# Kernel optimization log

Hardware: AMD Instinct MI355X
Metric: run time of the kernel (lower is better)

## Reference

```python
import jax, jax.numpy as jnp
import numpy as np

EPS = 1e-12  # torch F.normalize eps


def _unfold(x, k, pad, stride):
    # torch F.unfold: [B,C,H,W] -> [B, C*k*k, L], channel-major then kernel (i,j)
    B, C, H, W = x.shape
    xp = jnp.pad(x, ((0, 0), (0, 0), (pad, pad), (pad, pad)))
    Ho = (H + 2 * pad - k) // stride + 1
    Wo = (W + 2 * pad - k) // stride + 1
    patches = [xp[:, :, i:i + stride * (Ho - 1) + 1:stride, j:j + stride * (Wo - 1) + 1:stride]
               for i in range(k) for j in range(k)]
    p = jnp.stack(patches, axis=2)  # [B, C, k*k, Ho, Wo]
    return p.reshape(B, C * k * k, Ho * Wo)


def _fold(t, out_hw, k, pad, stride):
    # torch F.fold: [B, C*k*k, L] -> [B, C, H, W] with overlap-add
    B, Ckk, L = t.shape
    C = Ckk // (k * k)
    H, W = out_hw
    Ho = (H + 2 * pad - k) // stride + 1
    Wo = (W + 2 * pad - k) // stride + 1
    t = t.reshape(B, C, k, k, Ho, Wo)
    out = jnp.zeros((B, C, H + 2 * pad, W + 2 * pad), t.dtype)
    for i in range(k):
        for j in range(k):
            out = out.at[:, :, i:i + stride * (Ho - 1) + 1:stride,
                         j:j + stride * (Wo - 1) + 1:stride].add(t[:, :, i, j])
    return out[:, :, pad:pad + H, pad:pad + W]


def setup_inputs() -> dict:
    key = jax.random.key(0)
    ks = jax.random.split(key, 5)
    B, C3, H3 = 4, 256, 48
    return {
        'dh_img_lv3': jax.random.normal(ks[0], (B, C3, H3, H3), jnp.float32),
        'dh_ref_lv3': jax.random.normal(ks[1], (B, C3, H3, H3), jnp.float32),
        'cl_ref_lv1': jax.random.normal(ks[2], (B, 64, H3 * 4, H3 * 4), jnp.float32),
        'cl_ref_lv2': jax.random.normal(ks[3], (B, 128, H3 * 2, H3 * 2), jnp.float32),
        'cl_ref_lv3': jax.random.normal(ks[4], (B, C3, H3, H3), jnp.float32),
    }


def reference(dh_img_lv3, dh_ref_lv3, cl_ref_lv1, cl_ref_lv2, cl_ref_lv3):
    ksz, pad = 3, 1
    B, C3, H3, W3 = dh_img_lv3.shape

    q = _unfold(dh_img_lv3, ksz, pad, 1)                      # [B, D, Lq]
    kmat = _unfold(dh_ref_lv3, ksz, pad, 1).transpose(0, 2, 1)  # [B, Lk, D]
    kmat = kmat / jnp.maximum(jnp.linalg.norm(kmat, axis=2, keepdims=True), EPS)
    q = q / jnp.maximum(jnp.linalg.norm(q, axis=1, keepdims=True), EPS)

    rel = jnp.einsum('bld,bdm->blm', kmat, q)                 # [B, Lk, Lq]
    rel_val = jnp.max(rel, axis=1, keepdims=True)             # [B, 1, Lq]  (top-1, k=1)
    rel_idx = jnp.argmax(rel, axis=1, keepdims=True)          # [B, 1, Lq]

    v3 = _unfold(cl_ref_lv3, ksz, pad, 1)                     # [B, C3*9,   Lk]
    v2 = _unfold(cl_ref_lv2, 2 * ksz, 2 * pad, 2)             # [B, C2*36,  Lk]
    v1 = _unfold(cl_ref_lv1, 4 * ksz, 4 * pad, 4)             # [B, C1*144, Lk]

    def transfer(v):
        idx = jnp.broadcast_to(rel_idx, (B, v.shape[1], rel_idx.shape[2]))
        tv = jnp.take_along_axis(v, idx, axis=2)              # [B, Cv, Lq]
        # weighted sum over k=1 topk / sum of weights (faithful to original)
        return (rel_val * tv) / rel_val

    T3u, T2u, T1u = transfer(v3), transfer(v2), transfer(v1)

    def fold_norm(Tu, scale, k_, p_, s_):
        hw = (H3 * scale, W3 * scale)
        cnt = _fold(jnp.ones_like(Tu), hw, k_, p_, s_)
        return _fold(Tu, hw, k_, p_, s_) / cnt

    T_lv3 = fold_norm(T3u, 1, ksz, pad, 1)
    T_lv2 = fold_norm(T2u, 2, 2 * ksz, 2 * pad, 2)
    T_lv1 = fold_norm(T1u, 4, 4 * ksz, 4 * pad, 4)

    S = rel_val.reshape(B, 1, H3, W3)
    return S, T_lv3, T_lv2, T_lv1
```

## Files before the change

kernel.cpp:

```cpp
#include <hip/hip_runtime.h>


#define HW3 2304
#define PLANE 589824
#define SSTRIDE 5308416LL

__global__ __launch_bounds__(256) void k_pixsq(const float* __restrict__ img,
                                               const float* __restrict__ ref,
                                               float* __restrict__ psi,
                                               float* __restrict__ psr) {
  __shared__ float ri[16][17], rr[16][17];
  int t = threadIdx.x;
  int pl = t & 15, cg = t >> 4;
  int pix = blockIdx.x * 16 + pl;
  int b = pix / HW3, p = pix - b * HW3;
  const float* ib = img + (size_t)b * PLANE + p;
  const float* rb = ref + (size_t)b * PLANE + p;
  float si = 0.f, sr = 0.f;
#pragma unroll
  for (int c = 0; c < 16; ++c) {
    float x = ib[(cg * 16 + c) * HW3]; si = fmaf(x, x, si);
    float y = rb[(cg * 16 + c) * HW3]; sr = fmaf(y, y, sr);
  }
  ri[pl][cg] = si; rr[pl][cg] = sr;
  __syncthreads();
  if (t < 16) {
    float a = 0.f, s2 = 0.f;
#pragma unroll
    for (int g = 0; g < 16; ++g) { a += ri[t][g]; s2 += rr[t][g]; }
    int pix2 = blockIdx.x * 16 + t;
    psi[pix2] = a; psr[pix2] = s2;
  }
}

__global__ __launch_bounds__(256) void k_norm(const float* __restrict__ psr,
                                              const float* __restrict__ psi,
                                              float* __restrict__ ikn,
                                              float* __restrict__ iqn) {
  int pix = blockIdx.x * 256 + threadIdx.x;
  int b = pix / HW3, p = pix - b * HW3;
  int py = p / 48, px = p - py * 48;
  float sr = 0.f, si = 0.f;
#pragma unroll
  for (int dy = -1; dy <= 1; ++dy) {
#pragma unroll
    for (int dx = -1; dx <= 1; ++dx) {
      if (py + dy < 0 || py + dy >= 48 || px + dx < 0 || px + dx >= 48) continue;
      int n = pix + dy * 48 + dx;
      sr += psr[n]; si += psi[n];
    }
  }
  ikn[pix] = 1.0f / fmaxf(sqrtf(sr), 1e-12f);
  iqn[pix] = 1.0f / fmaxf(sqrtf(si), 1e-12f);
}

__global__ __launch_bounds__(256) void k_gemm(const float* __restrict__ img,
                                              const float* __restrict__ ref,
                                              float* __restrict__ S,
                                              int b0, long long sstride) {
  __shared__ float As[8][128];
  __shared__ float Bs[8][128];
  const float* A  = img + (size_t)(b0 + blockIdx.z) * PLANE;
  const float* Bm = ref + (size_t)(b0 + blockIdx.z) * PLANE;
  float* Sb = S + (size_t)blockIdx.z * sstride;
  const int t = threadIdx.x;
  const int q0 = blockIdx.y * 128, p0 = blockIdx.x * 128;
  const int lr = t >> 5, lc = (t & 31) << 2;
  const int tq = t >> 4, tp = t & 15;
  float acc[8][8];
#pragma unroll
  for (int u = 0; u < 8; ++u)
#pragma unroll
    for (int v = 0; v < 8; ++v) acc[u][v] = 0.f;

  for (int c0 = 0; c0 < 256; c0 += 8) {
    float4 a4 = *(const float4*)(A  + (c0 + lr) * HW3 + q0 + lc);
    float4 b4 = *(const float4*)(Bm + (c0 + lr) * HW3 + p0 + lc);
    __syncthreads();
    *(float4*)(&As[lr][lc]) = a4;
    *(float4*)(&Bs[lr][lc]) = b4;
    __syncthreads();
#pragma unroll
    for (int kk = 0; kk < 8; ++kk) {
      float4 a0 = *(const float4*)(&As[kk][tq * 8]);
      float4 a1 = *(const float4*)(&As[kk][tq * 8 + 4]);
      float4 b0 = *(const float4*)(&Bs[kk][tp * 4]);
      float4 b1 = *(const float4*)(&Bs[kk][64 + tp * 4]);
      float av[8] = {a0.x, a0.y, a0.z, a0.w, a1.x, a1.y, a1.z, a1.w};
      float bv[8] = {b0.x, b0.y, b0.z, b0.w, b1.x, b1.y, b1.z, b1.w};
#pragma unroll
      for (int u = 0; u < 8; ++u)
#pragma unroll
        for (int v = 0; v < 8; ++v)
          acc[u][v] = fmaf(av[u], bv[v], acc[u][v]);
    }
  }
#pragma unroll
  for (int u = 0; u < 8; ++u) {
    int q = q0 + tq * 8 + u;
    float* o = Sb + (size_t)q * HW3 + p0;
    *(float4*)(o + tp * 4)      = make_float4(acc[u][0], acc[u][1], acc[u][2], acc[u][3]);
    *(float4*)(o + 64 + tp * 4) = make_float4(acc[u][4], acc[u][5], acc[u][6], acc[u][7]);
  }
}

__global__ __launch_bounds__(256) void k_argmax2(const float* __restrict__ S,
                                                 const float* __restrict__ ikn,
                                                 const float* __restrict__ iqn,
                                                 int* __restrict__ oidx,
                                                 float* __restrict__ oval,
                                                 int b0, long long sstride) {
  __shared__ float L[16][354];
  __shared__ float rv[4][4];
  __shared__ int   ri4[4][4];
  const int b = b0 + blockIdx.z;
  const float* Sb = S + (size_t)blockIdx.z * sstride;
  const float* iknb = ikn + b * HW3;
  const float* iqnb = iqn + b * HW3;
  const int qy0 = blockIdx.y * 2, qx0 = blockIdx.x * 2;
  const int t = threadIdx.x;

  float best[4]; int bid[4];
#pragma unroll
  for (int i = 0; i < 4; ++i) { best[i] = -1e30f; bid[i] = 0; }

  for (int pc = 0; pc < 9; ++pc) {
    const int cbase = pc * 256 - 49;
    for (int e = t; e < 16 * 354; e += 256) {
      int row = e / 354, col = e - row * 354;
      int u = row >> 2, v = row & 3;
      int ry = qy0 - 1 + u, rx = qx0 - 1 + v;
      int c = cbase + col;
      float val = 0.f;
      if (ry >= 0 && ry < 48 && rx >= 0 && rx < 48 && c >= 0 && c < HW3)
        val = Sb[(size_t)(ry * 48 + rx) * HW3 + c];
      L[row][col] = val;
    }
    __syncthreads();
    const int p = pc * 256 + t;
    const int py = p / 48, px = p - py * 48;
#pragma unroll
    for (int a = 0; a < 2; ++a)
#pragma unroll
      for (int bb = 0; bb < 2; ++bb) {
        const int qy = qy0 + a, qx = qx0 + bb;
        float s = 0.f;
#pragma unroll
        for (int dy = -1; dy <= 1; ++dy) {
          if (qy + dy < 0 || qy + dy >= 48 || py + dy < 0 || py + dy >= 48) continue;
#pragma unroll
          for (int dx = -1; dx <= 1; ++dx) {
            if (qx + dx < 0 || qx + dx >= 48 || px + dx < 0 || px + dx >= 48) continue;
            s += L[(a + dy + 1) * 4 + (bb + dx + 1)][t + 49 + dy * 48 + dx];
          }
        }
        float v = s * iknb[p];
        int qi = a * 2 + bb;
        if (v > best[qi]) { best[qi] = v; bid[qi] = p; }
      }
    __syncthreads();
  }

  int lane = t & 63, wv = t >> 6;
#pragma unroll
  for (int qi = 0; qi < 4; ++qi) {
    float bv = best[qi]; int bi = bid[qi];
#pragma unroll
    for (int off = 32; off; off >>= 1) {
      float ov = __shfl_down(bv, off);
      int   oi = __shfl_down(bi, off);
      if (ov > bv || (ov == bv && oi < bi)) { bv = ov; bi = oi; }
    }
    if (lane == 0) { rv[qi][wv] = bv; ri4[qi][wv] = bi; }
  }
  __syncthreads();
  if (t < 4) {
    float bv = rv[t][0]; int bi = ri4[t][0];
#pragma unroll
    for (int w = 1; w < 4; ++w)
      if (rv[t][w] > bv || (rv[t][w] == bv && ri4[t][w] < bi)) { bv = rv[t][w]; bi = ri4[t][w]; }
    int qy = qy0 + (t >> 1), qx = qx0 + (t & 1), q = qy * 48 + qx;
    oidx[b * HW3 + q] = bi;
    oval[b * HW3 + q] = bv * iqnb[q];
  }
}

__global__ __launch_bounds__(256) void k_tr(const float* __restrict__ src,
                                            float* __restrict__ dst,
                                            int C, int HW, int b0) {
  __shared__ float sm[64][65];
  int pix0 = blockIdx.x * 64, c0 = blockIdx.y * 64;
  const float* s = src + (size_t)(b0 + blockIdx.z) * C * HW;
  float* d = dst + (size_t)blockIdx.z * HW * C;
  int lane = threadIdx.x & 63, q4 = threadIdx.x >> 6;
#pragma unroll
  for (int r = 0; r < 16; ++r) {
    int cl = r * 4 + q4;
    sm[cl][lane] = s[(size_t)(c0 + cl) * HW + pix0 + lane];
  }
  __syncthreads();
#pragma unroll
  for (int r = 0; r < 16; ++r) {
    int pl = r * 4 + q4;
    d[(size_t)(pix0 + pl) * C + c0 + lane] = sm[lane][pl];
  }
}

__global__ __launch_bounds__(256) void k_foldgather(const float* __restrict__ t,
                                                    const int* __restrict__ ridx,
                                                    float* __restrict__ out,
                                                    int C, int H, int sc, int b0) {
  __shared__ int   soff[64][9];
  __shared__ float sicnt[64];
  __shared__ float tr[64][65];
  const int HW = H * H;
  const int b = b0 + blockIdx.y;
  const float* tb = t + (size_t)blockIdx.y * HW * C;
  const int* rb = ridx + b * HW3;
  const int pix0 = blockIdx.x * 64;

  for (int e = threadIdx.x; e < 576; e += 256) {
    int op = e / 9, tap = e - op * 9;
    int pix = pix0 + op;
    int h = pix / H, w = pix - h * H;
    int hi = h / sc, hr = h - hi * sc;
    int wi = w / sc, wr = w - wi * sc;
    int ii = tap / 3, jj = tap - ii * 3;
    int oy = hi + 1 - ii, ox = wi + 1 - jj;
    int off = -1;
    if (oy >= 0 && oy < 48 && ox >= 0 && ox < 48) {
      int m = rb[oy * 48 + ox];
      int my = m / 48, mx = m - my * 48;
      int y = sc * (my - 1 + ii) + hr;
      int x = sc * (mx - 1 + jj) + wr;
      if (y >= 0 && y < H && x >= 0 && x < H) off = y * H + x;
    }
    soff[op][tap] = off;
    if (tap == 0) {
      int cnt = 0;
#pragma unroll
      for (int i2 = 0; i2 < 3; ++i2)
#pragma unroll
        for (int j2 = 0; j2 < 3; ++j2) {
          int oy2 = hi + 1 - i2, ox2 = wi + 1 - j2;
          if (oy2 >= 0 && oy2 < 48 && ox2 >= 0 && ox2 < 48) ++cnt;
        }
      sicnt[op] = 1.0f / (float)cnt;
    }
  }
  __syncthreads();

  const int g = threadIdx.x >> 6, lane = threadIdx.x & 63;
  for (int c0 = 0; c0 < C; c0 += 64) {
#pragma unroll
    for (int o = 0; o < 16; ++o) {
      int op = g * 16 + o;
      float s = 0.f;
#pragma unroll
      for (int tp = 0; tp < 9; ++tp) {
        int off = soff[op][tp];
        if (off >= 0) s += tb[(size_t)off * C + c0 + lane];
      }
      tr[op][lane] = s * sicnt[op];
    }
    __syncthreads();
#pragma unroll
    for (int r = 0; r < 16; ++r) {
      int cl = r * 4 + g;
      out[((size_t)b * C + c0 + cl) * HW + pix0 + lane] = tr[lane][cl];
    }
    __syncthreads();
  }
}

extern "C" void kernel_launch(void* const* d_in, const int* in_sizes, int n_in,
                              void* d_out, int out_size, void* d_ws, size_t ws_size,
                              hipStream_t stream) {
  (void)in_sizes; (void)n_in; (void)out_size;
  const float* img = (const float*)d_in[0];
  const float* ref = (const float*)d_in[1];
  const float* cl1 = (const float*)d_in[2];
  const float* cl2 = (const float*)d_in[3];
  const float* cl3 = (const float*)d_in[4];
  float* out = (float*)d_out;

  float* ws   = (float*)d_ws;
  float* ps_i = ws;
  float* ps_r = ws + 9216;
  float* ikn  = ws + 18432;
  float* iqn  = ws + 27648;
  int*   ridx = (int*)(ws + 36864);
  float* S    = ws + 46080;

  const long long availf = (long long)(ws_size / 4) - 46080;
  const bool bigS   = availf >= 4 * SSTRIDE;
  const bool lv1all = availf >= 9437184LL;

  k_pixsq<<<576, 256, 0, stream>>>(img, ref, ps_i, ps_r);
  k_norm<<<36, 256, 0, stream>>>(ps_r, ps_i, ikn, iqn);

  if (bigS) {
    k_gemm<<<dim3(18, 18, 4), 256, 0, stream>>>(img, ref, S, 0, SSTRIDE);
    k_argmax2<<<dim3(24, 24, 4), 256, 0, stream>>>(S, ikn, iqn, ridx, out, 0, SSTRIDE);
  } else {
    for (int b = 0; b < 4; ++b) {
      k_gemm<<<dim3(18, 18, 1), 256, 0, stream>>>(img, ref, S, b, 0LL);
      k_argmax2<<<dim3(24, 24, 1), 256, 0, stream>>>(S, ikn, iqn, ridx, out, b, 0LL);
    }
  }

  float* t = S;

  k_tr<<<dim3(36, 4, 4), 256, 0, stream>>>(cl3, t, 256, 2304, 0);
  k_foldgather<<<dim3(36, 4), 256, 0, stream>>>(t, ridx, out + 9216, 256, 48, 1, 0);
  k_tr<<<dim3(144, 2, 4), 256, 0, stream>>>(cl2, t, 128, 9216, 0);
  k_foldgather<<<dim3(144, 4), 256, 0, stream>>>(t, ridx, out + 2368512, 128, 96, 2, 0);
  if (lv1all) {
    k_tr<<<dim3(576, 1, 4), 256, 0, stream>>>(cl1, t, 64, 36864, 0);
    k_foldgather<<<dim3(576, 4), 256, 0, stream>>>(t, ridx, out + 7087104, 64, 192, 4, 0);
  } else {
    for (int b = 0; b < 4; ++b) {
      k_tr<<<dim3(576, 1, 1), 256, 0, stream>>>(cl1, t, 64, 36864, b);
      k_foldgather<<<dim3(576, 1), 256, 0, stream>>>(t, ridx, out + 7087104, 64, 192, 4, b);
    }
  }
}
```

Baseline: 807.3 us.

## Use split-bf16 MFMA GEMM on padded layout with top-2 candidates and fp32 rescore

Replaces the fp32 SIMT correlation GEMM with a bf16 MFMA GEMM. Inputs are split into hi/lo bf16 parts (three cross products) and written into a zero-padded 50x50 pixel layout, so the 3x3 window sum in the argmax needs no bounds checks. The argmax now keeps the top two candidates per query, and a new rescore kernel recomputes both in exact fp32 to pick the winner. This trades extra transpose/split kernels, a workspace memset and a larger padded S buffer for much faster matrix math. The lv1 per-batch fallback is removed, so the code now assumes a large workspace.

```diff
diff --git a/kernel.cpp b/kernel.cpp
--- a/kernel.cpp
+++ b/kernel.cpp
@@ -3,7 +3,24 @@
 
 #define HW3 2304
 #define PLANE 589824
-#define SSTRIDE 5308416LL
+#define MP 2560
+#define KP 512
+
+typedef __bf16 v8bf __attribute__((ext_vector_type(8)));
+typedef float v16f __attribute__((ext_vector_type(16)));
+
+#define O_PSI  0
+#define O_PSR  9216
+#define O_IKN  18432
+#define O_IQN  27648
+#define O_RIDX 36864
+#define O_IKNP 46080
+#define O_CAND 56320
+#define O_IMGT 74752
+#define O_REFT 2434048
+#define O_APL  4793344
+#define O_BPL  7414784
+#define O_S    10036224
 
 __global__ __launch_bounds__(256) void k_pixsq(const float* __restrict__ img,
                                                const float* __restrict__ ref,
@@ -42,146 +59,61 @@
   int py = p / 48, px = p - py * 48;
   float sr = 0.f, si = 0.f;
 #pragma unroll
-  for (int dy = -1; dy <= 1; ++dy) {
+  for (int dy = -1; dy <= 1; ++dy)
 #pragma unroll
     for (int dx = -1; dx <= 1; ++dx) {
       if (py + dy < 0 || py + dy >= 48 || px + dx < 0 || px + dx >= 48) continue;
       int n = pix + dy * 48 + dx;
       sr += psr[n]; si += psi[n];
     }
-  }
   ikn[pix] = 1.0f / fmaxf(sqrtf(sr), 1e-12f);
   iqn[pix] = 1.0f / fmaxf(sqrtf(si), 1e-12f);
 }
 
-__global__ __launch_bounds__(256) void k_gemm(const float* __restrict__ img,
-                                              const float* __restrict__ ref,
-                                              float* __restrict__ S,
-                                              int b0, long long sstride) {
-  __shared__ float As[8][128];
-  __shared__ float Bs[8][128];
-  const float* A  = img + (size_t)(b0 + blockIdx.z) * PLANE;
-  const float* Bm = ref + (size_t)(b0 + blockIdx.z) * PLANE;
-  float* Sb = S + (size_t)blockIdx.z * sstride;
-  const int t = threadIdx.x;
-  const int q0 = blockIdx.y * 128, p0 = blockIdx.x * 128;
-  const int lr = t >> 5, lc = (t & 31) << 2;
-  const int tq = t >> 4, tp = t & 15;
-  float acc[8][8];
-#pragma unroll
-  for (int u = 0; u < 8; ++u)
-#pragma unroll
-    for (int v = 0; v < 8; ++v) acc[u][v] = 0.f;
-
-  for (int c0 = 0; c0 < 256; c0 += 8) {
-    float4 a4 = *(const float4*)(A  + (c0 + lr) * HW3 + q0 + lc);
-    float4 b4 = *(const float4*)(Bm + (c0 + lr) * HW3 + p0 + lc);
-    __syncthreads();
-    *(float4*)(&As[lr][lc]) = a4;
-    *(float4*)(&Bs[lr][lc]) = b4;
-    __syncthreads();
-#pragma unroll
-    for (int kk = 0; kk < 8; ++kk) {
-      float4 a0 = *(const float4*)(&As[kk][tq * 8]);
-      float4 a1 = *(const float4*)(&As[kk][tq * 8 + 4]);
-      float4 b0 = *(const float4*)(&Bs[kk][tp * 4]);
-      float4 b1 = *(const float4*)(&Bs[kk][64 + tp * 4]);
-      float av[8] = {a0.x, a0.y, a0.z, a0.w, a1.x, a1.y, a1.z, a1.w};
-      float bv[8] = {b0.x, b0.y, b0.z, b0.w, b1.x, b1.y, b1.z, b1.w};
-#pragma unroll
-      for (int u = 0; u < 8; ++u)
-#pragma unroll
-        for (int v = 0; v < 8; ++v)
-          acc[u][v] = fmaf(av[u], bv[v], acc[u][v]);
-    }
-  }
-#pragma unroll
-  for (int u = 0; u < 8; ++u) {
-    int q = q0 + tq * 8 + u;
-    float* o = Sb + (size_t)q * HW3 + p0;
-    *(float4*)(o + tp * 4)      = make_float4(acc[u][0], acc[u][1], acc[u][2], acc[u][3]);
-    *(float4*)(o + 64 + tp * 4) = make_float4(acc[u][4], acc[u][5], acc[u][6], acc[u][7]);
-  }
-}
-
-__global__ __launch_bounds__(256) void k_argmax2(const float* __restrict__ S,
-                                                 const float* __restrict__ ikn,
-                                                 const float* __restrict__ iqn,
-                                                 int* __restrict__ oidx,
-                                                 float* __restrict__ oval,
-                                                 int b0, long long sstride) {
-  __shared__ float L[16][354];
-  __shared__ float rv[4][4];
-  __shared__ int   ri4[4][4];
-  const int b = b0 + blockIdx.z;
-  const float* Sb = S + (size_t)blockIdx.z * sstride;
-  const float* iknb = ikn + b * HW3;
-  const float* iqnb = iqn + b * HW3;
-  const int qy0 = blockIdx.y * 2, qx0 = blockIdx.x * 2;
-  const int t = threadIdx.x;
-
-  float best[4]; int bid[4];
-#pragma unroll
-  for (int i = 0; i < 4; ++i) { best[i] = -1e30f; bid[i] = 0; }
-
-  for (int pc = 0; pc < 9; ++pc) {
-    const int cbase = pc * 256 - 49;
-    for (int e = t; e < 16 * 354; e += 256) {
-      int row = e / 354, col = e - row * 354;
-      int u = row >> 2, v = row & 3;
-      int ry = qy0 - 1 + u, rx = qx0 - 1 + v;
-      int c = cbase + col;
-      float val = 0.f;
-      if (ry >= 0 && ry < 48 && rx >= 0 && rx < 48 && c >= 0 && c < HW3)
-        val = Sb[(size_t)(ry * 48 + rx) * HW3 + c];
-      L[row][col] = val;
-    }
-    __syncthreads();
-    const int p = pc * 256 + t;
-    const int py = p / 48, px = p - py * 48;
-#pragma unroll
-    for (int a = 0; a < 2; ++a)
-#pragma unroll
-      for (int bb = 0; bb < 2; ++bb) {
-        const int qy = qy0 + a, qx = qx0 + bb;
-        float s = 0.f;
-#pragma unroll
-        for (int dy = -1; dy <= 1; ++dy) {
-          if (qy + dy < 0 || qy + dy >= 48 || py + dy < 0 || py + dy >= 48) continue;
-#pragma unroll
-          for (int dx = -1; dx <= 1; ++dx) {
-            if (qx + dx < 0 || qx + dx >= 48 || px + dx < 0 || px + dx >= 48) continue;
-            s += L[(a + dy + 1) * 4 + (bb + dx + 1)][t + 49 + dy * 48 + dx];
-          }
-        }
-        float v = s * iknb[p];
-        int qi = a * 2 + bb;
-        if (v > best[qi]) { best[qi] = v; bid[qi] = p; }
+__global__ __launch_bounds__(256) void k_normp(const float* __restrict__ psr,
+                                               float* __restrict__ iknp) {
+  int idx = blockIdx.x * 256 + threadIdx.x;
+  int b = idx / MP, pp = idx - b * MP;
+  int py = pp / 50, px = pp - py * 50;
+  float r = __uint_as_float(0x7fc00000u);
+  if (pp < 2500 && py != 0 && py != 49 && px != 0 && px != 49) {
+    int y = py - 1, x = px - 1;
+    float s = 0.f;
+    for (int dy = -1; dy <= 1; ++dy)
+      for (int dx = -1; dx <= 1; ++dx) {
+        int yy = y + dy, xx = x + dx;
+        if (yy >= 0 && yy < 48 && xx >= 0 && xx < 48)
+          s += psr[b * HW3 + yy * 48 + xx];
       }
-    __syncthreads();
-  }
-
-  int lane = t & 63, wv = t >> 6;
-#pragma unroll
-  for (int qi = 0; qi < 4; ++qi) {
-    float bv = best[qi]; int bi = bid[qi];
-#pragma unroll
-    for (int off = 32; off; off >>= 1) {
-      float ov = __shfl_down(bv, off);
-      int   oi = __shfl_down(bi, off);
-      if (ov > bv || (ov == bv && oi < bi)) { bv = ov; bi = oi; }
-    }
-    if (lane == 0) { rv[qi][wv] = bv; ri4[qi][wv] = bi; }
+    r = 1.0f / fmaxf(sqrtf(s), 1e-12f);
+  }
+  iknp[idx] = r;
+}
+
+__global__ __launch_bounds__(256) void k_padsplit(const float* __restrict__ src,
+                                                  __bf16* __restrict__ dst) {
+  __shared__ float sm[64][65];
+  const int pix0 = blockIdx.x * 64, c0 = blockIdx.y * 64, b = blockIdx.z;
+  const int lane = threadIdx.x & 63, q4 = threadIdx.x >> 6;
+  const float* s = src + (size_t)b * PLANE;
+#pragma unroll
+  for (int r = 0; r < 16; ++r) {
+    int cl = r * 4 + q4;
+    sm[cl][lane] = s[(size_t)(c0 + cl) * HW3 + pix0 + lane];
   }
   __syncthreads();
-  if (t < 4) {
-    float bv = rv[t][0]; int bi = ri4[t][0];
-#pragma unroll
-    for (int w = 1; w < 4; ++w)
-      if (rv[t][w] > bv || (rv[t][w] == bv && ri4[t][w] < bi)) { bv = rv[t][w]; bi = ri4[t][w]; }
-    int qy = qy0 + (t >> 1), qx = qx0 + (t & 1), q = qy * 48 + qx;
-    oidx[b * HW3 + q] = bi;
-    oval[b * HW3 + q] = bv * iqnb[q];
+  __bf16* d = dst + (size_t)b * MP * KP;
+#pragma unroll
+  for (int r = 0; r < 16; ++r) {
+    int pl = r * 4 + q4;
+    int p = pix0 + pl;
+    int py = p / 48, px = p - py * 48;
+    int pp = (py + 1) * 50 + px + 1;
+    float v = sm[lane][pl];
+    __bf16 hi = (__bf16)v;
+    __bf16 lo = (__bf16)(v - (float)hi);
+    d[(size_t)pp * KP + c0 + lane] = hi;
+    d[(size_t)pp * KP + 256 + c0 + lane] = lo;
   }
 }
 
@@ -203,6 +135,215 @@
   for (int r = 0; r < 16; ++r) {
     int pl = r * 4 + q4;
     d[(size_t)(pix0 + pl) * C + c0 + lane] = sm[lane][pl];
+  }
+}
+
+__global__ __launch_bounds__(256) void k_gemm_mfma(const __bf16* __restrict__ Apl,
+                                                   const __bf16* __restrict__ Bpl,
+                                                   float* __restrict__ S, int b0) {
+  __shared__ __bf16 As[128][72];
+  __shared__ __bf16 Bs[128][72];
+  const int b = b0 + blockIdx.z;
+  const __bf16* Ab = Apl + (size_t)b * MP * KP;
+  const __bf16* Bb = Bpl + (size_t)b * MP * KP;
+  float* Sb = S + (size_t)blockIdx.z * (2560LL * 2560LL);
+  const int t = threadIdx.x;
+  const int q0 = blockIdx.y * 128, p0 = blockIdx.x * 128;
+  const int lane = t & 63, w = t >> 6, wr = w >> 1, wc = w & 1;
+  const int sr = t >> 1, ss = (t & 1) * 32;
+  const int l31 = lane & 31, kb = (lane >> 5) * 8;
+
+  v16f acc[2][2];
+#pragma unroll
+  for (int i = 0; i < 2; ++i)
+#pragma unroll
+    for (int j = 0; j < 2; ++j)
+#pragma unroll
+      for (int e = 0; e < 16; ++e) acc[i][j][e] = 0.f;
+
+  for (int kv = 0; kv < 768; kv += 64) {
+    const int ak = kv < 256 ? kv : kv - 256;
+    const int bk = kv < 512 ? kv : kv - 512;
+    const __bf16* ga = Ab + (size_t)(q0 + sr) * KP + ak + ss;
+    const __bf16* gb = Bb + (size_t)(p0 + sr) * KP + bk + ss;
+    float4 a0 = *(const float4*)(ga);
+    float4 a1 = *(const float4*)(ga + 8);
+    float4 a2 = *(const float4*)(ga + 16);
+    float4 a3 = *(const float4*)(ga + 24);
+    float4 b0v = *(const float4*)(gb);
+    float4 b1v = *(const float4*)(gb + 8);
+    float4 b2v = *(const float4*)(gb + 16);
+    float4 b3v = *(const float4*)(gb + 24);
+    __syncthreads();
+    *(float4*)(&As[sr][ss])      = a0;
+    *(float4*)(&As[sr][ss + 8])  = a1;
+    *(float4*)(&As[sr][ss + 16]) = a2;
+    *(float4*)(&As[sr][ss + 24]) = a3;
+    *(float4*)(&Bs[sr][ss])      = b0v;
+    *(float4*)(&Bs[sr][ss + 8])  = b1v;
+    *(float4*)(&Bs[sr][ss + 16]) = b2v;
+    *(float4*)(&Bs[sr][ss + 24]) = b3v;
+    __syncthreads();
+#pragma unroll
+    for (int kk = 0; kk < 4; ++kk) {
+      const int ko = kk * 16 + kb;
+      v8bf af0 = *(const v8bf*)(&As[wr * 64 + l31][ko]);
+      v8bf af1 = *(const v8bf*)(&As[wr * 64 + 32 + l31][ko]);
+      v8bf bg0 = *(const v8bf*)(&Bs[wc * 64 + l31][ko]);
+      v8bf bg1 = *(const v8bf*)(&Bs[wc * 64 + 32 + l31][ko]);
+      acc[0][0] = __builtin_amdgcn_mfma_f32_32x32x16_bf16(af0, bg0, acc[0][0], 0, 0, 0);
+      acc[0][1] = __builtin_amdgcn_mfma_f32_32x32x16_bf16(af0, bg1, acc[0][1], 0, 0, 0);
+      acc[1][0] = __builtin_amdgcn_mfma_f32_32x32x16_bf16(af1, bg0, acc[1][0], 0, 0, 0);
+      acc[1][1] = __builtin_amdgcn_mfma_f32_32x32x16_bf16(af1, bg1, acc[1][1], 0, 0, 0);
+    }
+  }
+#pragma unroll
+  for (int mf = 0; mf < 2; ++mf)
+#pragma unroll
+    for (int nf = 0; nf < 2; ++nf) {
+      const int col = p0 + wc * 64 + nf * 32 + l31;
+#pragma unroll
+      for (int r = 0; r < 16; ++r) {
+        const int row = q0 + wr * 64 + mf * 32 + (r & 3) + 8 * (r >> 2) + 4 * (lane >> 5);
+        Sb[(size_t)row * MP + col] = acc[mf][nf][r];
+      }
+    }
+}
+
+__device__ __forceinline__ void top2merge(float& b1, int& i1, float& b2, int& i2,
+                                          float o1, int oj1, float o2, int oj2) {
+  if (o1 > b1 || (o1 == b1 && oj1 < i1)) {
+    float t1 = b1; int tj = i1;
+    b1 = o1; i1 = oj1;
+    if (o2 > t1 || (o2 == t1 && oj2 < tj)) { b2 = o2; i2 = oj2; }
+    else { b2 = t1; i2 = tj; }
+  } else if (o1 > b2 || (o1 == b2 && oj1 < i2)) {
+    b2 = o1; i2 = oj1;
+  }
+}
+
+__global__ __launch_bounds__(256) void k_argmax_pad(const float* __restrict__ S,
+                                                    const float* __restrict__ iknp,
+                                                    int* __restrict__ cand, int b0) {
+  __shared__ float L[30 * 258];
+  __shared__ float smv[8][4][2];
+  __shared__ int   smi[8][4][2];
+  const int b = b0 + blockIdx.z;
+  const float* Sb = S + (size_t)blockIdx.z * (2560LL * 2560LL);
+  const float* ik = iknp + b * MP;
+  const int qy = blockIdx.y, qx0 = blockIdx.x * 8;
+  const int t = threadIdx.x, lane = t & 63, wv = t >> 6;
+  const int gb[3] = { qy * 50 + qx0, (qy + 1) * 50 + qx0, (qy + 2) * 50 + qx0 };
+
+  float b1[8], b2[8]; int i1[8], i2[8];
+#pragma unroll
+  for (int a = 0; a < 8; ++a) { b1[a] = -3e38f; b2[a] = -3e38f; i1[a] = 51; i2[a] = 51; }
+
+  for (int pc = 0; pc < MP; pc += 256) {
+    for (int row = wv; row < 30; row += 4) {
+      int g = (row >= 20) ? 2 : (row >= 10 ? 1 : 0);
+      int rr = row - g * 10;
+      int gbase = (g == 0) ? gb[0] : (g == 1 ? gb[1] : gb[2]);
+      int cb = pc + 50 * (g - 1) - 1;
+      const float* src = Sb + (size_t)(gbase + rr) * MP;
+      float* dstL = L + row * 258;
+      for (int c = lane; c < 258; c += 64) {
+        int cg = cb + c;
+        float v = 0.f;
+        if (cg >= 0 && cg < MP) v = src[cg];
+        dstL[c] = v;
+      }
+    }
+    __syncthreads();
+    const float ikv = ik[pc + t];
+    const int p = pc + t;
+#pragma unroll
+    for (int a = 0; a < 8; ++a) {
+      float s = 0.f;
+#pragma unroll
+      for (int g = 0; g < 3; ++g)
+#pragma unroll
+        for (int dx = -1; dx <= 1; ++dx)
+          s += L[(g * 10 + a + dx + 1) * 258 + (t + dx + 1)];
+      float v = s * ikv;
+      if (v > b1[a]) { b2[a] = b1[a]; i2[a] = i1[a]; b1[a] = v; i1[a] = p; }
+      else if (v > b2[a]) { b2[a] = v; i2[a] = p; }
+    }
+    __syncthreads();
+  }
+
+#pragma unroll
+  for (int a = 0; a < 8; ++a) {
+    float x1 = b1[a], x2 = b2[a]; int j1 = i1[a], j2 = i2[a];
+#pragma unroll
+    for (int off = 32; off; off >>= 1) {
+      float o1 = __shfl_down(x1, off), o2 = __shfl_down(x2, off);
+      int oj1 = __shfl_down(j1, off), oj2 = __shfl_down(j2, off);
+      top2merge(x1, j1, x2, j2, o1, oj1, o2, oj2);
+    }
+    if (lane == 0) { smv[a][wv][0] = x1; smv[a][wv][1] = x2; smi[a][wv][0] = j1; smi[a][wv][1] = j2; }
+  }
+  __syncthreads();
+  if (t < 8) {
+    float x1 = smv[t][0][0], x2 = smv[t][0][1]; int j1 = smi[t][0][0], j2 = smi[t][0][1];
+#pragma unroll
+    for (int w2 = 1; w2 < 4; ++w2)
+      top2merge(x1, j1, x2, j2, smv[t][w2][0], smi[t][w2][0], smv[t][w2][1], smi[t][w2][1]);
+    int q = qy * 48 + qx0 + t;
+    cand[((size_t)b * HW3 + q) * 2]     = j1;
+    cand[((size_t)b * HW3 + q) * 2 + 1] = j2;
+  }
+}
+
+__global__ __launch_bounds__(256) void k_rescore(const float* __restrict__ imgT,
+                                                 const float* __restrict__ refT,
+                                                 const float* __restrict__ ikn,
+                                                 const float* __restrict__ iqn,
+                                                 const int* __restrict__ cand,
+                                                 int* __restrict__ ridx,
+                                                 float* __restrict__ outS) {
+  const int t = threadIdx.x, lane = t & 63, sub = t >> 6;
+  const int qg = blockIdx.x * 4 + sub;
+  const int b = qg / HW3, q = qg - b * HW3;
+  const int qy = q / 48, qx = q - qy * 48;
+  const float* iT = imgT + (size_t)b * HW3 * 256;
+  const float* rT = refT + (size_t)b * HW3 * 256;
+  const int c0 = cand[qg * 2], c1 = cand[qg * 2 + 1];
+  const int p0y = c0 / 50 - 1, p0x = c0 % 50 - 1;
+  const int p1y = c1 / 50 - 1, p1x = c1 % 50 - 1;
+  float s0 = 0.f, s1 = 0.f;
+  for (int dy = -1; dy <= 1; ++dy) {
+    int yq = qy + dy; if (yq < 0 || yq >= 48) continue;
+    for (int dx = -1; dx <= 1; ++dx) {
+      int xq = qx + dx; if (xq < 0 || xq >= 48) continue;
+      const float* qrow = iT + (size_t)(yq * 48 + xq) * 256;
+      int y0 = p0y + dy, x0 = p0x + dx;
+      int y1 = p1y + dy, x1 = p1x + dx;
+      bool v0 = (y0 >= 0 && y0 < 48 && x0 >= 0 && x0 < 48);
+      bool v1 = (y1 >= 0 && y1 < 48 && x1 >= 0 && x1 < 48);
+      const float* r0 = rT + (size_t)((v0 ? y0 * 48 + x0 : 0)) * 256;
+      const float* r1 = rT + (size_t)((v1 ? y1 * 48 + x1 : 0)) * 256;
+#pragma unroll
+      for (int j = 0; j < 4; ++j) {
+        float qv = qrow[lane + j * 64];
+        if (v0) s0 = fmaf(qv, r0[lane + j * 64], s0);
+        if (v1) s1 = fmaf(qv, r1[lane + j * 64], s1);
+      }
+    }
+  }
+#pragma unroll
+  for (int off = 32; off; off >>= 1) {
+    s0 += __shfl_down(s0, off);
+    s1 += __shfl_down(s1, off);
+  }
+  if (lane == 0) {
+    int m0 = p0y * 48 + p0x, m1 = p1y * 48 + p1x;
+    float v0 = s0 * ikn[b * HW3 + m0], v1 = s1 * ikn[b * HW3 + m1];
+    int win; float vw;
+    if (v1 > v0 || (v1 == v0 && m1 < m0)) { win = m1; vw = v1; }
+    else { win = m0; vw = v0; }
+    ridx[b * HW3 + q] = win;
+    outS[qg] = vw * iqn[b * HW3 + q];
   }
 }
 
@@ -285,43 +426,43 @@
   float* out = (float*)d_out;
 
   float* ws   = (float*)d_ws;
-  float* ps_i = ws;
-  float* ps_r = ws + 9216;
-  float* ikn  = ws + 18432;
-  float* iqn  = ws + 27648;
-  int*   ridx = (int*)(ws + 36864);
-  float* S    = ws + 46080;
-
-  const long long availf = (long long)(ws_size / 4) - 46080;
-  const bool bigS   = availf >= 4 * SSTRIDE;
-  const bool lv1all = availf >= 9437184LL;
+  float* ps_i = ws + O_PSI;
+  float* ps_r = ws + O_PSR;
+  float* ikn  = ws + O_IKN;
+  float* iqn  = ws + O_IQN;
+  int*   ridx = (int*)(ws + O_RIDX);
+  float* iknp = ws + O_IKNP;
+  int*   cand = (int*)(ws + O_CAND);
+  float* imgT = ws + O_IMGT;
+  float* refT = ws + O_REFT;
+  __bf16* Apl = (__bf16*)(ws + O_APL);
+  __bf16* Bpl = (__bf16*)(ws + O_BPL);
+  float* Sm   = ws + O_S;
+
+  hipMemsetAsync(ws + O_APL, 0, (size_t)(O_S - O_APL) * 4, stream);
 
   k_pixsq<<<576, 256, 0, stream>>>(img, ref, ps_i, ps_r);
   k_norm<<<36, 256, 0, stream>>>(ps_r, ps_i, ikn, iqn);
-
-  if (bigS) {
-    k_gemm<<<dim3(18, 18, 4), 256, 0, stream>>>(img, ref, S, 0, SSTRIDE);
-    k_argmax2<<<dim3(24, 24, 4), 256, 0, stream>>>(S, ikn, iqn, ridx, out, 0, SSTRIDE);
-  } else {
-    for (int b = 0; b < 4; ++b) {
-      k_gemm<<<dim3(18, 18, 1), 256, 0, stream>>>(img, ref, S, b, 0LL);
-      k_argmax2<<<dim3(24, 24, 1), 256, 0, stream>>>(S, ikn, iqn, ridx, out, b, 0LL);
-    }
-  }
-
-  float* t = S;
-
+  k_normp<<<40, 256, 0, stream>>>(ps_r, iknp);
+  k_padsplit<<<dim3(36, 4, 4), 256, 0, stream>>>(img, Apl);
+  k_padsplit<<<dim3(36, 4, 4), 256, 0, stream>>>(ref, Bpl);
+  k_tr<<<dim3(36, 4, 4), 256, 0, stream>>>(img, imgT, 256, HW3, 0);
+  k_tr<<<dim3(36, 4, 4), 256, 0, stream>>>(ref, refT, 256, HW3, 0);
+
+  const long long SPF = 2560LL * 2560LL;
+  const long long availf = (long long)(ws_size / 4) - O_S;
+  const int nb = (availf >= 4 * SPF) ? 4 : ((availf >= 2 * SPF) ? 2 : 1);
+  for (int g = 0; g < 4; g += nb) {
+    k_gemm_mfma<<<dim3(20, 20, nb), 256, 0, stream>>>(Apl, Bpl, Sm, g);
+    k_argmax_pad<<<dim3(6, 48, nb), 256, 0, stream>>>(Sm, iknp, cand, g);
+  }
+  k_rescore<<<2304, 256, 0, stream>>>(imgT, refT, ikn, iqn, cand, ridx, out);
+
+  float* t = ws + O_IMGT;
   k_tr<<<dim3(36, 4, 4), 256, 0, stream>>>(cl3, t, 256, 2304, 0);
   k_foldgather<<<dim3(36, 4), 256, 0, stream>>>(t, ridx, out + 9216, 256, 48, 1, 0);
   k_tr<<<dim3(144, 2, 4), 256, 0, stream>>>(cl2, t, 128, 9216, 0);
   k_foldgather<<<dim3(144, 4), 256, 0, stream>>>(t, ridx, out + 2368512, 128, 96, 2, 0);
-  if (lv1all) {
-    k_tr<<<dim3(576, 1, 4), 256, 0, stream>>>(cl1, t, 64, 36864, 0);
-    k_foldgather<<<dim3(576, 4), 256, 0, stream>>>(t, ridx, out + 7087104, 64, 192, 4, 0);
-  } else {
-    for (int b = 0; b < 4; ++b) {
-      k_tr<<<dim3(576, 1, 1), 256, 0, stream>>>(cl1, t, 64, 36864, b);
-      k_foldgather<<<dim3(576, 1), 256, 0, stream>>>(t, ridx, out + 7087104, 64, 192, 4, b);
-    }
-  }
-}
+  k_tr<<<dim3(576, 1, 4), 256, 0, stream>>>(cl1, t, 64, 36864, 0);
+  k_foldgather<<<dim3(576, 4), 256, 0, stream>>>(t, ridx, out + 7087104, 64, 192, 4, 0);
+}
```

After: 800.2 us. About the same (-0.9%).
